# Kernel optimization log

Measured on AMD Instinct MI355X. Metric: run time of the kernel, lower is better.

The kernel has to match this reference:

```python
import jax, jax.numpy as jnp
import numpy as np

N, C, H, W = 4, 256, 128, 128
BLOCK = 8
FWB = H // BLOCK  # feature_size_with_block = 16
N_BBOX = 100
M = N_BBOX * N * FWB * FWB  # 102400 rois


def setup_inputs() -> dict:
    key = jax.random.key(0)
    ks = jax.random.split(key, 6)
    s = 1.0 / np.sqrt(C).astype(np.float32)
    return {
        "feature": jax.random.normal(ks[0], (N, C, H, W), jnp.float32),
        "rois_feature": jax.random.normal(ks[1], (M, C, 1, 1), jnp.float32),
        "W_weight": jax.random.normal(ks[2], (C, C), jnp.float32) * s,
        "b_weight": jnp.zeros((C,), jnp.float32),
        "W_fuse": jax.random.normal(ks[3], (C, C), jnp.float32) * s,
        "b_fuse": jnp.zeros((C,), jnp.float32),
        "W_pw": jax.random.normal(ks[4], (BLOCK * BLOCK, C), jnp.float32) * s,
        "b_pw": jnp.zeros((BLOCK * BLOCK,), jnp.float32),
        "feature_size_with_block": FWB,
    }


def reference(feature, rois_feature, W_weight, b_weight, W_fuse, b_fuse, W_pw, b_pw, feature_size_with_block):
    n, c, h, w = feature.shape
    f = feature_size_with_block
    blk = h // f  # block_size
    m = rois_feature.shape[0]
    n_bbox = m // (n * f * f)

    x = rois_feature[:, :, 0, 0]  # [M, C] (1x1 conv on 1x1 spatial == dense layer)
    feat_w = jax.nn.relu(x @ W_weight.T + b_weight)  # [M, C]
    feat_f = jax.nn.relu(x @ W_fuse.T + b_fuse)      # [M, C]
    point_weight = feat_w @ W_pw.T + b_pw            # [M, B*B]

    # [n_bbox, N, F, F, B, B] -> [N, n_bbox, F, F, B, B]
    pw = point_weight.reshape(n_bbox, n, f, f, blk, blk).transpose(1, 0, 2, 3, 4, 5)
    # feature -> blocks: [N, C, F, B, F, B] -> [N, C, F, F, B, B]
    fb = feature.reshape(n, c, f, blk, f, blk).transpose(0, 1, 2, 4, 3, 5)
    # weighted block-sum without materializing the n_bbox-repeated tensor.
    # torch: sum over (B,B) -> [N,nb,C,F,F], then permute(1,0,3,4,2) -> [nb,N,F,F,C]
    out = jnp.einsum('ncpqab,nkpqab->knpqc', fb, pw)  # [nb, N, F, F, C]
    out = out.reshape(m, c)[:, :, None, None]          # [M, C, 1, 1]
    fused = feat_f[:, :, None, None] + out
    return fused, out
```

## Files before the change

kernel.cpp:

```cpp
#include <hip/hip_runtime.h>

#define NN 4
#define CC 256
#define HH 128
#define FWBv 16
#define BLK 8
#define NBBOX 100
#define MM (NBBOX * NN * FWBv * FWBv)

typedef __attribute__((ext_vector_type(8))) short bf16x8;
typedef __attribute__((ext_vector_type(4))) float f32x4;

__device__ __forceinline__ unsigned short f2bf(float x) {
  union { float f; unsigned int u; } v; v.f = x;
  unsigned int r = v.u + 0x7FFFu + ((v.u >> 16) & 1u);
  return (unsigned short)(r >> 16);
}

__global__ __launch_bounds__(256) void k_convert(
    const float* __restrict__ Wf, const float* __restrict__ Ww,
    const float* __restrict__ Wpw,
    unsigned short* __restrict__ oWf, unsigned short* __restrict__ oWw,
    unsigned short* __restrict__ oWpw) {
  int i = blockIdx.x * 256 + threadIdx.x;
  oWf[i] = f2bf(Wf[i]);
  oWw[i] = f2bf(Ww[i]);
  if (i < 64 * 256) oWpw[i] = f2bf(Wpw[i]);
}

__device__ __forceinline__ void gemm_k256(
    const unsigned short (*xs)[264], const unsigned short* __restrict__ B,
    int w, int lr, int quad, f32x4 acc[4][4]) {
#pragma unroll
  for (int kt = 0; kt < 8; ++kt) {
    const int kk = kt * 32 + quad * 8;
    bf16x8 a[4], b[4];
#pragma unroll
    for (int mt = 0; mt < 4; ++mt)
      a[mt] = *(const bf16x8*)&xs[mt * 16 + lr][kk];
#pragma unroll
    for (int nt = 0; nt < 4; ++nt)
      b[nt] = *(const bf16x8*)(B + (size_t)(w * 64 + nt * 16 + lr) * 256 + kk);
#pragma unroll
    for (int mt = 0; mt < 4; ++mt)
#pragma unroll
      for (int nt = 0; nt < 4; ++nt)
        acc[mt][nt] = __builtin_amdgcn_mfma_f32_16x16x32_bf16(
            a[mt], b[nt], acc[mt][nt], 0, 0, 0);
  }
}

__global__ __launch_bounds__(256) void k1(
    const float* __restrict__ rois,
    const unsigned short* __restrict__ Wf,
    const unsigned short* __restrict__ Ww,
    const unsigned short* __restrict__ Wpw,
    const float* __restrict__ bf_, const float* __restrict__ bw_,
    const float* __restrict__ bpw_,
    float* __restrict__ fused_slot,
    float* __restrict__ out_slot)
{
  __shared__ unsigned short xs[64][264];
  const int t = threadIdx.x;
  const int lane = t & 63, w = t >> 6;
  const int lr = lane & 15, quad = lane >> 4;
  const int row_base = blockIdx.x * 64;

#pragma unroll
  for (int i = 0; i < 16; ++i) {
    const int elem = (i * 256 + t) * 4;
    const int r = elem >> 8, c = elem & 255;
    const float4 v = *(const float4*)(rois + (size_t)row_base * 256 + elem);
    unsigned int lo = f2bf(v.x) | ((unsigned int)f2bf(v.y) << 16);
    unsigned int hi = f2bf(v.z) | ((unsigned int)f2bf(v.w) << 16);
    *(uint2*)&xs[r][c] = make_uint2(lo, hi);
  }
  __syncthreads();

  {
    f32x4 acc[4][4];
#pragma unroll
    for (int mt = 0; mt < 4; ++mt)
#pragma unroll
      for (int nt = 0; nt < 4; ++nt) acc[mt][nt] = (f32x4){0.f, 0.f, 0.f, 0.f};
    gemm_k256(xs, Wf, w, lr, quad, acc);
#pragma unroll
    for (int nt = 0; nt < 4; ++nt) {
      const int gcol = w * 64 + nt * 16 + lr;
      const float bias = bf_[gcol];
#pragma unroll
      for (int mt = 0; mt < 4; ++mt)
#pragma unroll
        for (int r = 0; r < 4; ++r) {
          float vv = acc[mt][nt][r] + bias;
          vv = vv > 0.f ? vv : 0.f;
          fused_slot[(size_t)(row_base + mt * 16 + quad * 4 + r) * 256 + gcol] = vv;
        }
    }
  }

  {
    f32x4 acc[4][4];
#pragma unroll
    for (int mt = 0; mt < 4; ++mt)
#pragma unroll
      for (int nt = 0; nt < 4; ++nt) acc[mt][nt] = (f32x4){0.f, 0.f, 0.f, 0.f};
    gemm_k256(xs, Ww, w, lr, quad, acc);
    __syncthreads();
#pragma unroll
    for (int nt = 0; nt < 4; ++nt) {
      const int gcol = w * 64 + nt * 16 + lr;
      const float bias = bw_[gcol];
#pragma unroll
      for (int mt = 0; mt < 4; ++mt)
#pragma unroll
        for (int r = 0; r < 4; ++r) {
          float vv = acc[mt][nt][r] + bias;
          vv = vv > 0.f ? vv : 0.f;
          xs[mt * 16 + quad * 4 + r][gcol] = f2bf(vv);
        }
    }
    __syncthreads();
  }

  {
    f32x4 acc2[4];
#pragma unroll
    for (int mt = 0; mt < 4; ++mt) acc2[mt] = (f32x4){0.f, 0.f, 0.f, 0.f};
#pragma unroll
    for (int kt = 0; kt < 8; ++kt) {
      const int kk = kt * 32 + quad * 8;
      const bf16x8 b = *(const bf16x8*)(Wpw + (size_t)(w * 16 + lr) * 256 + kk);
#pragma unroll
      for (int mt = 0; mt < 4; ++mt) {
        const bf16x8 a = *(const bf16x8*)&xs[mt * 16 + lr][kk];
        acc2[mt] = __builtin_amdgcn_mfma_f32_16x16x32_bf16(a, b, acc2[mt], 0, 0, 0);
      }
    }
    const int j = w * 16 + lr;
    const float bias = bpw_[j];
#pragma unroll
    for (int mt = 0; mt < 4; ++mt)
#pragma unroll
      for (int r = 0; r < 4; ++r)
        out_slot[(size_t)(row_base + mt * 16 + quad * 4 + r) * 256 + j] =
            acc2[mt][r] + bias;
  }
}

__global__ __launch_bounds__(512) void k2(
    const float* __restrict__ feature,
    float* __restrict__ fused_slot,
    float* __restrict__ out_slot)
{
  __shared__ unsigned short fbuf[256][72];
  __shared__ unsigned short pwb[112][72];
  const int t = threadIdx.x;
  const int lane = t & 63, w = t >> 6;
  const int lr = lane & 15, quad = lane >> 4;
  const int bid = blockIdx.x;
  const int n = bid >> 8, p = (bid >> 4) & 15, q = bid & 15;

  if (t < 432) {
    const int r = 100 + t / 36, cw = t % 36;
    *(unsigned int*)&pwb[r][cw * 2] = 0u;
  }

  for (int pi = t; pi < 2048; pi += 512) {
    const int c = pi >> 3, a = pi & 7;
    const float* fp =
        feature + (((size_t)n * 256 + c) * 128 + p * 8 + a) * 128 + q * 8;
    const float4 v0 = *(const float4*)fp;
    const float4 v1 = *(const float4*)(fp + 4);
    unsigned int u0 = f2bf(v0.x) | ((unsigned int)f2bf(v0.y) << 16);
    unsigned int u1 = f2bf(v0.z) | ((unsigned int)f2bf(v0.w) << 16);
    unsigned int u2 = f2bf(v1.x) | ((unsigned int)f2bf(v1.y) << 16);
    unsigned int u3 = f2bf(v1.z) | ((unsigned int)f2bf(v1.w) << 16);
    *(uint4*)&fbuf[c][a * 8] = make_uint4(u0, u1, u2, u3);
  }

  for (int pi = t; pi < 1600; pi += 512) {
    const int k = pi >> 4, ch = pi & 15;
    const float4 v =
        *(const float4*)(out_slot + (size_t)(bid + k * 1024) * 256 + ch * 4);
    unsigned int lo = f2bf(v.x) | ((unsigned int)f2bf(v.y) << 16);
    unsigned int hi = f2bf(v.z) | ((unsigned int)f2bf(v.w) << 16);
    *(uint2*)&pwb[k][ch * 4] = make_uint2(lo, hi);
  }
  __syncthreads();

  f32x4 acc[7][2];
#pragma unroll
  for (int mt = 0; mt < 7; ++mt)
#pragma unroll
    for (int nt = 0; nt < 2; ++nt) acc[mt][nt] = (f32x4){0.f, 0.f, 0.f, 0.f};
#pragma unroll
  for (int kt = 0; kt < 2; ++kt) {
    const int kk = kt * 32 + quad * 8;
    bf16x8 a[7], b[2];
#pragma unroll
    for (int mt = 0; mt < 7; ++mt)
      a[mt] = *(const bf16x8*)&pwb[mt * 16 + lr][kk];
#pragma unroll
    for (int nt = 0; nt < 2; ++nt)
      b[nt] = *(const bf16x8*)&fbuf[w * 32 + nt * 16 + lr][kk];
#pragma unroll
    for (int mt = 0; mt < 7; ++mt)
#pragma unroll
      for (int nt = 0; nt < 2; ++nt)
        acc[mt][nt] =
            __builtin_amdgcn_mfma_f32_16x16x32_bf16(a[mt], b[nt], acc[mt][nt], 0, 0, 0);
  }

#pragma unroll
  for (int mt = 0; mt < 7; ++mt) {
#pragma unroll
    for (int r = 0; r < 4; ++r) {
      const int k = mt * 16 + quad * 4 + r;
      if (k < 100) {
        const size_t rowoff = (size_t)(bid + k * 1024) * 256;
#pragma unroll
        for (int nt = 0; nt < 2; ++nt) {
          const int c = w * 32 + nt * 16 + lr;
          const float val = acc[mt][nt][r];
          out_slot[rowoff + c] = val;
          fused_slot[rowoff + c] = fused_slot[rowoff + c] + val;
        }
      }
    }
  }
}

extern "C" void kernel_launch(void* const* d_in, const int* in_sizes, int n_in,
                              void* d_out, int out_size, void* d_ws, size_t ws_size,
                              hipStream_t stream) {
  const float* feature = (const float*)d_in[0];
  const float* rois = (const float*)d_in[1];
  const float* Ww = (const float*)d_in[2];
  const float* bw = (const float*)d_in[3];
  const float* Wf = (const float*)d_in[4];
  const float* bfv = (const float*)d_in[5];
  const float* Wpw = (const float*)d_in[6];
  const float* bpw = (const float*)d_in[7];

  unsigned short* wsWf = (unsigned short*)d_ws;
  unsigned short* wsWw = wsWf + 256 * 256;
  unsigned short* wsWpw = wsWw + 256 * 256;

  float* fused_slot = (float*)d_out;
  float* out_slot = fused_slot + (size_t)MM * 256;

  k_convert<<<256, 256, 0, stream>>>(Wf, Ww, Wpw, wsWf, wsWw, wsWpw);
  k1<<<MM / 64, 256, 0, stream>>>(rois, wsWf, wsWw, wsWpw, bfv, bw, bpw,
                                  fused_slot, out_slot);
  k2<<<NN * FWBv * FWBv, 512, 0, stream>>>(feature, fused_slot, out_slot);
}
```

Before: 505.6 us.

## Stage k1 weight tiles into LDS via async global_load_lds

In k1, the Wf/Ww weights are now loaded cooperatively into a 32KB shared buffer in 64-wide K chunks using global-to-LDS async loads. MFMA operands then come from LDS instead of per-wave direct global loads. The Wpw weights for the final projection are staged the same way. The aim is to replace scattered global B-operand reads with coalesced async copies. In exchange it adds barriers per K chunk with no double buffering, and roughly doubles shared memory per block, which can lower occupancy.

After: 504.8 us. About the same (-0.2%).

```diff
diff --git a/kernel.cpp b/kernel.cpp
--- a/kernel.cpp
+++ b/kernel.cpp
@@ -15,6 +15,12 @@
   union { float f; unsigned int u; } v; v.f = x;
   unsigned int r = v.u + 0x7FFFu + ((v.u >> 16) & 1u);
   return (unsigned short)(r >> 16);
+}
+
+__device__ __forceinline__ void async16(const void* g, void* l) {
+  __builtin_amdgcn_global_load_lds(
+      (__attribute__((address_space(1))) void*)(g),
+      (__attribute__((address_space(3))) void*)(l), 16, 0, 0);
 }
 
 __global__ __launch_bounds__(256) void k_convert(
@@ -26,28 +32,6 @@
   oWf[i] = f2bf(Wf[i]);
   oWw[i] = f2bf(Ww[i]);
   if (i < 64 * 256) oWpw[i] = f2bf(Wpw[i]);
-}
-
-__device__ __forceinline__ void gemm_k256(
-    const unsigned short (*xs)[264], const unsigned short* __restrict__ B,
-    int w, int lr, int quad, f32x4 acc[4][4]) {
-#pragma unroll
-  for (int kt = 0; kt < 8; ++kt) {
-    const int kk = kt * 32 + quad * 8;
-    bf16x8 a[4], b[4];
-#pragma unroll
-    for (int mt = 0; mt < 4; ++mt)
-      a[mt] = *(const bf16x8*)&xs[mt * 16 + lr][kk];
-#pragma unroll
-    for (int nt = 0; nt < 4; ++nt)
-      b[nt] = *(const bf16x8*)(B + (size_t)(w * 64 + nt * 16 + lr) * 256 + kk);
-#pragma unroll
-    for (int mt = 0; mt < 4; ++mt)
-#pragma unroll
-      for (int nt = 0; nt < 4; ++nt)
-        acc[mt][nt] = __builtin_amdgcn_mfma_f32_16x16x32_bf16(
-            a[mt], b[nt], acc[mt][nt], 0, 0, 0);
-  }
 }
 
 __global__ __launch_bounds__(256) void k1(
@@ -61,6 +45,7 @@
     float* __restrict__ out_slot)
 {
   __shared__ unsigned short xs[64][264];
+  __shared__ unsigned short bs[256 * 64];
   const int t = threadIdx.x;
   const int lane = t & 63, w = t >> 6;
   const int lr = lane & 15, quad = lane >> 4;
@@ -75,62 +60,91 @@
     unsigned int hi = f2bf(v.z) | ((unsigned int)f2bf(v.w) << 16);
     *(uint2*)&xs[r][c] = make_uint2(lo, hi);
   }
-  __syncthreads();
+
+  for (int pass = 0; pass < 2; ++pass) {
+    const unsigned short* Wp = pass ? Ww : Wf;
+    f32x4 acc[4][4];
+#pragma unroll
+    for (int mt = 0; mt < 4; ++mt)
+#pragma unroll
+      for (int nt = 0; nt < 4; ++nt) acc[mt][nt] = (f32x4){0.f, 0.f, 0.f, 0.f};
+
+    for (int kc = 0; kc < 4; ++kc) {
+      __syncthreads();
+#pragma unroll
+      for (int i = 0; i < 8; ++i) {
+        const int r0 = i * 32 + w * 8;
+        const unsigned short* g =
+            Wp + (size_t)(r0 + (lane >> 3)) * 256 + kc * 64 + (lane & 7) * 8;
+        async16(g, &bs[r0 * 64]);
+      }
+      __syncthreads();
+#pragma unroll
+      for (int kt = 0; kt < 2; ++kt) {
+        const int kk = kt * 32 + quad * 8;
+        bf16x8 a[4], b[4];
+#pragma unroll
+        for (int mt = 0; mt < 4; ++mt)
+          a[mt] = *(const bf16x8*)&xs[mt * 16 + lr][kc * 64 + kk];
+#pragma unroll
+        for (int nt = 0; nt < 4; ++nt)
+          b[nt] = *(const bf16x8*)&bs[(w * 64 + nt * 16 + lr) * 64 + kk];
+#pragma unroll
+        for (int mt = 0; mt < 4; ++mt)
+#pragma unroll
+          for (int nt = 0; nt < 4; ++nt)
+            acc[mt][nt] = __builtin_amdgcn_mfma_f32_16x16x32_bf16(
+                a[mt], b[nt], acc[mt][nt], 0, 0, 0);
+      }
+    }
+
+    if (pass == 0) {
+#pragma unroll
+      for (int nt = 0; nt < 4; ++nt) {
+        const int gcol = w * 64 + nt * 16 + lr;
+        const float bias = bf_[gcol];
+#pragma unroll
+        for (int mt = 0; mt < 4; ++mt)
+#pragma unroll
+          for (int r = 0; r < 4; ++r) {
+            float vv = acc[mt][nt][r] + bias;
+            vv = vv > 0.f ? vv : 0.f;
+            fused_slot[(size_t)(row_base + mt * 16 + quad * 4 + r) * 256 + gcol] = vv;
+          }
+      }
+    } else {
+      __syncthreads();
+#pragma unroll
+      for (int nt = 0; nt < 4; ++nt) {
+        const int gcol = w * 64 + nt * 16 + lr;
+        const float bias = bw_[gcol];
+#pragma unroll
+        for (int mt = 0; mt < 4; ++mt)
+#pragma unroll
+          for (int r = 0; r < 4; ++r) {
+            float vv = acc[mt][nt][r] + bias;
+            vv = vv > 0.f ? vv : 0.f;
+            xs[mt * 16 + quad * 4 + r][gcol] = f2bf(vv);
+          }
+      }
+    }
+  }
 
   {
-    f32x4 acc[4][4];
-#pragma unroll
-    for (int mt = 0; mt < 4; ++mt)
-#pragma unroll
-      for (int nt = 0; nt < 4; ++nt) acc[mt][nt] = (f32x4){0.f, 0.f, 0.f, 0.f};
-    gemm_k256(xs, Wf, w, lr, quad, acc);
-#pragma unroll
-    for (int nt = 0; nt < 4; ++nt) {
-      const int gcol = w * 64 + nt * 16 + lr;
-      const float bias = bf_[gcol];
-#pragma unroll
-      for (int mt = 0; mt < 4; ++mt)
-#pragma unroll
-        for (int r = 0; r < 4; ++r) {
-          float vv = acc[mt][nt][r] + bias;
-          vv = vv > 0.f ? vv : 0.f;
-          fused_slot[(size_t)(row_base + mt * 16 + quad * 4 + r) * 256 + gcol] = vv;
-        }
-    }
-  }
-
-  {
-    f32x4 acc[4][4];
-#pragma unroll
-    for (int mt = 0; mt < 4; ++mt)
-#pragma unroll
-      for (int nt = 0; nt < 4; ++nt) acc[mt][nt] = (f32x4){0.f, 0.f, 0.f, 0.f};
-    gemm_k256(xs, Ww, w, lr, quad, acc);
+#pragma unroll
+    for (int i = 0; i < 8; ++i) {
+      const int off = (i * 4 + w) * 512;
+      async16((const void*)(Wpw + off + lane * 8), &bs[off]);
+    }
     __syncthreads();
-#pragma unroll
-    for (int nt = 0; nt < 4; ++nt) {
-      const int gcol = w * 64 + nt * 16 + lr;
-      const float bias = bw_[gcol];
-#pragma unroll
-      for (int mt = 0; mt < 4; ++mt)
-#pragma unroll
-        for (int r = 0; r < 4; ++r) {
-          float vv = acc[mt][nt][r] + bias;
-          vv = vv > 0.f ? vv : 0.f;
-          xs[mt * 16 + quad * 4 + r][gcol] = f2bf(vv);
-        }
-    }
-    __syncthreads();
-  }
-
-  {
+
     f32x4 acc2[4];
 #pragma unroll
     for (int mt = 0; mt < 4; ++mt) acc2[mt] = (f32x4){0.f, 0.f, 0.f, 0.f};
 #pragma unroll
     for (int kt = 0; kt < 8; ++kt) {
       const int kk = kt * 32 + quad * 8;
-      const bf16x8 b = *(const bf16x8*)(Wpw + (size_t)(w * 16 + lr) * 256 + kk);
+      const bf16x8 b = *(const bf16x8*)&bs[(w * 16 + lr) * 256 + kk];
 #pragma unroll
       for (int mt = 0; mt < 4; ++mt) {
         const bf16x8 a = *(const bf16x8*)&xs[mt * 16 + lr][kk];
```
